# Kernel optimization log

Hardware: AMD Instinct MI355X
Metric: run time of the kernel (lower is better)

Reference implementation:

```python
import jax, jax.numpy as jnp
import numpy as np

STEPS = 30
BATCH = 1048576
HIDDEN = 32


def setup_inputs() -> dict:
    key = jax.random.key(0)
    k_s, k_w1, k_b1, k_w2, k_b2 = jax.random.split(key, 5)
    return {
        "S": jax.random.normal(k_s, (BATCH, STEPS), dtype=jnp.float32),
        "W1": jax.random.normal(k_w1, (3, HIDDEN), dtype=jnp.float32) * (1.0 / np.sqrt(3.0)),
        "b1": jax.random.normal(k_b1, (HIDDEN,), dtype=jnp.float32) * 0.01,
        "W2": jax.random.normal(k_w2, (HIDDEN, 1), dtype=jnp.float32) * (1.0 / np.sqrt(HIDDEN)),
        "b2": jax.random.normal(k_b2, (1,), dtype=jnp.float32) * 0.01,
        "a_init": jnp.zeros((1,), dtype=jnp.float32),
    }


def reference(S, W1, b1, W2, b2, a_init):
    B = S.shape[0]
    h0 = jnp.zeros((B, 1), dtype=S.dtype)
    d0 = jnp.broadcast_to(a_init.reshape(1, 1), (B, 1))  # a_init.expand(batch, 1)

    def step(carry, s_t):
        h, d_prev = carry
        x = jnp.concatenate([s_t[:, None], d_prev, h], axis=1)  # (B, 3)
        hidden = jax.nn.relu(x @ W1 + b1)                        # (B, 32)
        d = hidden @ W2 + b2                                     # (B, 1)
        h_new = 0.8 * h + 0.2 * d
        return (h_new, d), d

    # scan over time: S.T has shape (steps, B)
    (_, _), deltas = jax.lax.scan(step, (h0, d0), S.T)
    # deltas: (steps, B, 1) -> (B, steps)
    return jnp.transpose(deltas[:, :, 0], (1, 0))
```

## Files before the change

kernel.cpp:

```cpp
#include <hip/hip_runtime.h>

#define STEPS 30
#define HID 32
#define HALF_H 16
#define NG 8
#define TPB 256
#define EPB (TPB / 2)
#define LDS_STRIDE (STEPS + 1)

typedef _Float16 h2 __attribute__((ext_vector_type(2)));

static __device__ __forceinline__ h2 pkrtz(float x, float y) {
    return __builtin_bit_cast(h2, __builtin_amdgcn_cvt_pkrtz(x, y));
}
static __device__ __forceinline__ h2 h2fma(h2 a, h2 b, h2 c) {
    return __builtin_elementwise_fma(a, b, c);
}
static __device__ __forceinline__ h2 h2max(h2 a, h2 b) {
    return __builtin_elementwise_max(a, b);
}

__global__ __launch_bounds__(TPB, 4) void hedge_kernel(
    const float* __restrict__ S,
    const float* __restrict__ W1,
    const float* __restrict__ b1,
    const float* __restrict__ W2,
    const float* __restrict__ b2,
    const float* __restrict__ a_init,
    float* __restrict__ out)
{
    __shared__ float tile[EPB * LDS_STRIDE];
    const int tid  = threadIdx.x;
    const int half = tid & 1;
    const int el   = tid >> 1;
    const long long base = (long long)blockIdx.x * (EPB * STEPS);

    #pragma unroll
    for (int k = 0; k < (EPB * STEPS) / TPB; ++k) {
        int idx = tid + k * TPB;
        float v = S[base + idx];
        int row = idx / STEPS;
        int col = idx - row * STEPS;
        tile[row * LDS_STRIDE + col] = v;
    }

    const int j0 = half * HALF_H;
    h2 wa[NG], wc[NG], we[NG], wb[NG], w2[NG];
    #pragma unroll
    for (int q = 0; q < 4; ++q) {
        float4 va = ((const float4*)(W1 + 0 * HID + j0))[q];
        float4 vc = ((const float4*)(W1 + 1 * HID + j0))[q];
        float4 ve = ((const float4*)(W1 + 2 * HID + j0))[q];
        float4 vb = ((const float4*)(b1 + j0))[q];
        float4 v2 = ((const float4*)(W2 + j0))[q];
        wa[2*q] = pkrtz(va.x, va.y); wa[2*q+1] = pkrtz(va.z, va.w);
        wc[2*q] = pkrtz(vc.x, vc.y); wc[2*q+1] = pkrtz(vc.z, vc.w);
        we[2*q] = pkrtz(ve.x, ve.y); we[2*q+1] = pkrtz(ve.z, ve.w);
        wb[2*q] = pkrtz(vb.x, vb.y); wb[2*q+1] = pkrtz(vb.z, vb.w);
        w2[2*q] = pkrtz(v2.x, v2.y); w2[2*q+1] = pkrtz(v2.z, v2.w);
    }
    const float bias2 = b2[0];
    float d = a_init[0];
    float h = 0.0f;
    const h2 zero2 = {(_Float16)0.0f, (_Float16)0.0f};
    __syncthreads();

    float* my = &tile[el * LDS_STRIDE];
    #pragma unroll
    for (int t = 0; t < STEPS; ++t) {
        const float s = my[t];
        const h2 s2 = pkrtz(s, s);
        const h2 d2 = pkrtz(d, d);
        const h2 h2v = pkrtz(h, h);
        float a0 = 0.f, a1 = 0.f, a2 = 0.f, a3 = 0.f;
        #pragma unroll
        for (int g = 0; g < NG; g += 4) {
            h2 t0 = h2fma(wa[g+0], s2, h2fma(wc[g+0], d2, h2fma(we[g+0], h2v, wb[g+0])));
            h2 t1 = h2fma(wa[g+1], s2, h2fma(wc[g+1], d2, h2fma(we[g+1], h2v, wb[g+1])));
            h2 t2 = h2fma(wa[g+2], s2, h2fma(wc[g+2], d2, h2fma(we[g+2], h2v, wb[g+2])));
            h2 t3 = h2fma(wa[g+3], s2, h2fma(wc[g+3], d2, h2fma(we[g+3], h2v, wb[g+3])));
            a0 = __builtin_amdgcn_fdot2(h2max(t0, zero2), w2[g+0], a0, false);
            a1 = __builtin_amdgcn_fdot2(h2max(t1, zero2), w2[g+1], a1, false);
            a2 = __builtin_amdgcn_fdot2(h2max(t2, zero2), w2[g+2], a2, false);
            a3 = __builtin_amdgcn_fdot2(h2max(t3, zero2), w2[g+3], a3, false);
        }
        float acc = (a0 + a1) + (a2 + a3);
        acc += __shfl_xor(acc, 1, 64);
        const float dn = bias2 + acc;
        h = fmaf(0.2f, dn, 0.8f * h);
        d = dn;
        if (!half) my[t] = dn;
    }
    __syncthreads();

    #pragma unroll
    for (int k = 0; k < (EPB * STEPS) / TPB; ++k) {
        int idx = tid + k * TPB;
        int row = idx / STEPS;
        int col = idx - row * STEPS;
        out[base + idx] = tile[row * LDS_STRIDE + col];
    }
}

extern "C" void kernel_launch(void* const* d_in, const int* in_sizes, int n_in,
                              void* d_out, int out_size, void* d_ws, size_t ws_size,
                              hipStream_t stream) {
    const float* S      = (const float*)d_in[0];
    const float* W1     = (const float*)d_in[1];
    const float* b1     = (const float*)d_in[2];
    const float* W2     = (const float*)d_in[3];
    const float* b2     = (const float*)d_in[4];
    const float* a_init = (const float*)d_in[5];
    float* out = (float*)d_out;

    const int batch = in_sizes[0] / STEPS;
    const int grid  = batch / EPB;
    hedge_kernel<<<grid, TPB, 0, stream>>>(S, W1, b1, W2, b2, a_init, out);
}
```

Baseline: 259.7 us.

## Assign one batch element per thread and drop cross-lane reduction shuffle

Each thread now evaluates all 32 hidden units for its own batch element, rather than splitting them across a lane pair. This removes the per-step shuffle and doubles the number of elements processed per thread. Blocks shrink to 64 threads, global loads and stores become float2, and the output bias is folded into the accumulator's initial value. The cost is a longer dependent chain per step and more registers holding weights, with less latency hiding from the smaller blocks. The launch-bounds value of 4 with 64-thread blocks may also limit occupancy.

Measured after the change: 273.1 us. 1.05x slower.

```diff
diff --git a/kernel.cpp b/kernel.cpp
--- a/kernel.cpp
+++ b/kernel.cpp
@@ -2,10 +2,9 @@
 
 #define STEPS 30
 #define HID 32
-#define HALF_H 16
-#define NG 8
-#define TPB 256
-#define EPB (TPB / 2)
+#define NG 16
+#define TPB 64
+#define EPB TPB
 #define LDS_STRIDE (STEPS + 1)
 
 typedef _Float16 h2 __attribute__((ext_vector_type(2)));
@@ -31,28 +30,27 @@
 {
     __shared__ float tile[EPB * LDS_STRIDE];
     const int tid  = threadIdx.x;
-    const int half = tid & 1;
-    const int el   = tid >> 1;
     const long long base = (long long)blockIdx.x * (EPB * STEPS);
 
+    const float2* S2 = (const float2*)(S + base);
     #pragma unroll
-    for (int k = 0; k < (EPB * STEPS) / TPB; ++k) {
-        int idx = tid + k * TPB;
-        float v = S[base + idx];
-        int row = idx / STEPS;
-        int col = idx - row * STEPS;
-        tile[row * LDS_STRIDE + col] = v;
+    for (int k = 0; k < (EPB * STEPS) / (2 * TPB); ++k) {
+        int i2 = tid + k * TPB;
+        float2 v = S2[i2];
+        int row = i2 / 15;
+        int col = 2 * (i2 - row * 15);
+        float* p = &tile[row * LDS_STRIDE + col];
+        p[0] = v.x; p[1] = v.y;
     }
 
-    const int j0 = half * HALF_H;
     h2 wa[NG], wc[NG], we[NG], wb[NG], w2[NG];
     #pragma unroll
-    for (int q = 0; q < 4; ++q) {
-        float4 va = ((const float4*)(W1 + 0 * HID + j0))[q];
-        float4 vc = ((const float4*)(W1 + 1 * HID + j0))[q];
-        float4 ve = ((const float4*)(W1 + 2 * HID + j0))[q];
-        float4 vb = ((const float4*)(b1 + j0))[q];
-        float4 v2 = ((const float4*)(W2 + j0))[q];
+    for (int q = 0; q < 8; ++q) {
+        float4 va = ((const float4*)(W1 + 0 * HID))[q];
+        float4 vc = ((const float4*)(W1 + 1 * HID))[q];
+        float4 ve = ((const float4*)(W1 + 2 * HID))[q];
+        float4 vb = ((const float4*)(b1))[q];
+        float4 v2 = ((const float4*)(W2))[q];
         wa[2*q] = pkrtz(va.x, va.y); wa[2*q+1] = pkrtz(va.z, va.w);
         wc[2*q] = pkrtz(vc.x, vc.y); wc[2*q+1] = pkrtz(vc.z, vc.w);
         we[2*q] = pkrtz(ve.x, ve.y); we[2*q+1] = pkrtz(ve.z, ve.w);
@@ -65,40 +63,40 @@
     const h2 zero2 = {(_Float16)0.0f, (_Float16)0.0f};
     __syncthreads();
 
-    float* my = &tile[el * LDS_STRIDE];
+    float* my = &tile[tid * LDS_STRIDE];
     #pragma unroll
     for (int t = 0; t < STEPS; ++t) {
         const float s = my[t];
-        const h2 s2 = pkrtz(s, s);
-        const h2 d2 = pkrtz(d, d);
+        const h2 s2v = pkrtz(s, s);
+        const h2 d2v = pkrtz(d, d);
         const h2 h2v = pkrtz(h, h);
-        float a0 = 0.f, a1 = 0.f, a2 = 0.f, a3 = 0.f;
+        float a0 = bias2, a1 = 0.f, a2 = 0.f, a3 = 0.f;
         #pragma unroll
         for (int g = 0; g < NG; g += 4) {
-            h2 t0 = h2fma(wa[g+0], s2, h2fma(wc[g+0], d2, h2fma(we[g+0], h2v, wb[g+0])));
-            h2 t1 = h2fma(wa[g+1], s2, h2fma(wc[g+1], d2, h2fma(we[g+1], h2v, wb[g+1])));
-            h2 t2 = h2fma(wa[g+2], s2, h2fma(wc[g+2], d2, h2fma(we[g+2], h2v, wb[g+2])));
-            h2 t3 = h2fma(wa[g+3], s2, h2fma(wc[g+3], d2, h2fma(we[g+3], h2v, wb[g+3])));
+            h2 t0 = h2fma(wa[g+0], s2v, h2fma(wc[g+0], d2v, h2fma(we[g+0], h2v, wb[g+0])));
+            h2 t1 = h2fma(wa[g+1], s2v, h2fma(wc[g+1], d2v, h2fma(we[g+1], h2v, wb[g+1])));
+            h2 t2 = h2fma(wa[g+2], s2v, h2fma(wc[g+2], d2v, h2fma(we[g+2], h2v, wb[g+2])));
+            h2 t3 = h2fma(wa[g+3], s2v, h2fma(wc[g+3], d2v, h2fma(we[g+3], h2v, wb[g+3])));
             a0 = __builtin_amdgcn_fdot2(h2max(t0, zero2), w2[g+0], a0, false);
             a1 = __builtin_amdgcn_fdot2(h2max(t1, zero2), w2[g+1], a1, false);
             a2 = __builtin_amdgcn_fdot2(h2max(t2, zero2), w2[g+2], a2, false);
             a3 = __builtin_amdgcn_fdot2(h2max(t3, zero2), w2[g+3], a3, false);
         }
-        float acc = (a0 + a1) + (a2 + a3);
-        acc += __shfl_xor(acc, 1, 64);
-        const float dn = bias2 + acc;
+        const float dn = (a0 + a1) + (a2 + a3);
         h = fmaf(0.2f, dn, 0.8f * h);
         d = dn;
-        if (!half) my[t] = dn;
+        my[t] = dn;
     }
     __syncthreads();
 
+    float2* O2 = (float2*)(out + base);
     #pragma unroll
-    for (int k = 0; k < (EPB * STEPS) / TPB; ++k) {
-        int idx = tid + k * TPB;
-        int row = idx / STEPS;
-        int col = idx - row * STEPS;
-        out[base + idx] = tile[row * LDS_STRIDE + col];
+    for (int k = 0; k < (EPB * STEPS) / (2 * TPB); ++k) {
+        int i2 = tid + k * TPB;
+        int row = i2 / 15;
+        int col = 2 * (i2 - row * 15);
+        const float* p = &tile[row * LDS_STRIDE + col];
+        O2[i2] = make_float2(p[0], p[1]);
     }
 }
 
```
